# Kernel optimization log

Measured on AMD Instinct MI355X. Metric: run time of the kernel, lower is better.

The kernel has to match this reference:

```python
import jax, jax.numpy as jnp
import numpy as np

B, N, H, FD = 2, 512, 128, 5
NT, SD, L = 3, 4, 3
COPY = 10.0
EPS = 1e-6


def setup_inputs() -> dict:
    key = jax.random.key(0)
    ks = jax.random.split(key, 20)
    node_type = jax.random.randint(ks[0], (B, N, 1), 0, NT).astype(jnp.float32)
    node_state = jax.random.normal(ks[1], (B, N, SD), jnp.float32)
    node_feats = jnp.concatenate([node_type, node_state], axis=-1)  # [B,N,5]
    adj = jax.random.bernoulli(ks[2], 0.05, (B, N, N)).astype(jnp.float32)
    adj = jnp.maximum(adj, adj.transpose(0, 2, 1)) * (1.0 - jnp.eye(N, dtype=jnp.float32))
    scope_node_mask = jax.random.bernoulli(ks[3], 0.5, (B, N)).astype(jnp.float32)
    scope_edge_mask = jax.random.bernoulli(ks[4], 0.5, (B, N, N)).astype(jnp.float32)
    s = 0.02
    p = dict(
        node_feats=node_feats, adj=adj,
        scope_node_mask=scope_node_mask, scope_edge_mask=scope_edge_mask,
        W_in=jax.random.normal(ks[5], (FD, H)) * s, b_in=jnp.zeros((H,)),
        W_mp=jax.random.normal(ks[6], (L, 2 * H, H)) * s, b_mp=jnp.zeros((L, H)),
        Wt1=jax.random.normal(ks[7], (H, H)) * s, bt1=jnp.zeros((H,)),
        Wt2=jax.random.normal(ks[8], (H, NT)) * s, bt2=jnp.zeros((NT,)),
        Ws1=jax.random.normal(ks[9], (H, H)) * s, bs1=jnp.zeros((H,)),
        Ws2=jax.random.normal(ks[10], (H, SD)) * s, bs2=jnp.zeros((SD,)),
        We1=jax.random.normal(ks[11], (4 * H, H)) * s, be1=jnp.zeros((H,)),
        We2=jax.random.normal(ks[12], (H, 3)) * s, be2=jnp.zeros((3,)),
    )
    return p


def _decode_edge_logits(adj, edl, eye):
    probs = jax.nn.softmax(edl, axis=-1)
    p_keep = probs[..., 0]  # EDGE_DELTA_KEEP = 0
    p_add = probs[..., 1]   # EDGE_DELTA_ADD = 1
    cur = (adj > 0.5).astype(edl.dtype)
    p_next = jnp.clip(p_add + p_keep * cur, EPS, 1.0 - EPS)
    el = jnp.log(p_next) - jnp.log1p(-p_next)  # logit
    return jnp.where(eye[None], -1e9, el)


def _forward(node_feats, adj, scope_node_mask, scope_edge_mask,
             W_in, b_in, W_mp, b_mp, Wt1, bt1, Wt2, bt2,
             Ws1, bs1, Ws2, bs2, We1, be1, We2, be2):
    # encoder: input proj + L rounds of [h, adj@h] -> Linear -> ReLU
    h = jax.nn.relu(node_feats @ W_in + b_in)  # [B,N,H]
    for l in range(L):
        msg = jnp.einsum('bij,bjh->bih', adj, h)
        h = jax.nn.relu(jnp.concatenate([h, msg], axis=-1) @ W_mp[l] + b_mp[l])
    # node heads (2-layer MLPs)
    type_local = jax.nn.relu(h @ Wt1 + bt1) @ Wt2 + bt2      # [B,N,NT]
    state_local = jax.nn.relu(h @ Ws1 + bs1) @ Ws2 + bs2     # [B,N,SD]
    # pairwise edge-delta head
    h_i = h[:, :, None, :]
    h_j = h[:, None, :, :]
    pair = jnp.concatenate([
        jnp.broadcast_to(h_i, (B, N, N, H)),
        jnp.broadcast_to(h_j, (B, N, N, H)),
        jnp.abs(h_i - h_j),
        h_i * h_j,
    ], axis=-1)  # [B,N,N,4H]
    edl = jax.nn.relu(pair @ We1 + be1) @ We2 + be2  # [B,N,N,3]
    edl = 0.5 * (edl + edl.transpose(0, 2, 1, 3))
    eye = jnp.eye(N, dtype=bool)
    edl = jnp.where(eye[None, :, :, None], 0.0, edl)
    # merges with copy paths
    cur_type = jnp.clip(node_feats[..., 0].astype(jnp.int32), 0, NT - 1)
    copy_type = jnp.where(jnp.arange(NT) == cur_type[..., None], COPY, -COPY)
    type_full = jnp.where(scope_node_mask[..., None] != 0, type_local, copy_type)
    scope = scope_node_mask[..., None]
    state_full = scope * state_local + (1.0 - scope) * node_feats[..., 1:]
    copy_edl = jnp.broadcast_to(jnp.where(jnp.arange(3) == 0, COPY, -COPY), (B, N, N, 3))
    copy_edl = jnp.where(eye[None, :, :, None], 0.0, copy_edl)
    edl_full = jnp.where(scope_edge_mask[..., None] != 0, edl, copy_edl)
    el_full = _decode_edge_logits(adj, edl_full, eye)
    return type_full, state_full, edl_full, el_full


def reference(node_feats, adj, scope_node_mask, scope_edge_mask,
              W_in, b_in, W_mp, b_mp, Wt1, bt1, Wt2, bt2,
              Ws1, bs1, Ws2, bs2, We1, be1, We2, be2):
    return _forward(node_feats, adj, scope_node_mask, scope_edge_mask,
                    W_in, b_in, W_mp, b_mp, Wt1, bt1, Wt2, bt2,
                    Ws1, bs1, Ws2, bs2, We1, be1, We2, be2)
```

## Files before the change

kernel.cpp:

```cpp
#include <hip/hip_runtime.h>
#include <math.h>

#define B_ 2
#define N_ 512
#define H_ 128
#define NT_ 3
#define SD_ 4
#define FD_ 5

typedef float f32x4 __attribute__((ext_vector_type(4)));
typedef unsigned int u32x4 __attribute__((ext_vector_type(4)));

#define MFMA16(acc, a, b) \
    asm("s_nop 1\n\tv_mfma_f32_16x16x32_bf16 %0, %1, %2, %0" \
        : "+v"(acc) : "v"(a), "v"(b))

#define CVTPK(d, a, b) \
    asm("v_cvt_pk_bf16_f32 %0, %1, %2" : "=v"(d) : "v"(a), "v"(b))

#define CVTPKA(d, a, b) \
    asm("v_cvt_pk_bf16_f32 %0, |%1|, |%2|" : "=v"(d) : "v"(a), "v"(b))

static __device__ inline unsigned rne1(float f) {
    unsigned u = __float_as_uint(f);
    u += 0x7fffu + ((u >> 16) & 1u);
    return u >> 16;
}

__global__ __launch_bounds__(128) void k_input(const float* __restrict__ feats,
                                               const float* __restrict__ W_in,
                                               const float* __restrict__ b_in,
                                               float* __restrict__ hout,
                                               const float* __restrict__ We1,
                                               const float* __restrict__ We2,
                                               unsigned short* __restrict__ wfrag,
                                               unsigned short* __restrict__ wfrag2) {
    int blk = blockIdx.x, tid = threadIdx.x;
    if (blk < B_ * N_) {
        const float* f = feats + (size_t)blk * FD_;
        float acc = b_in[tid];
#pragma unroll
        for (int k = 0; k < FD_; ++k) acc += f[k] * W_in[k * H_ + tid];
        hout[(size_t)blk * H_ + tid] = fmaxf(acc, 0.f);
        return;
    }
    if (blk < B_ * N_ + 32) {
        int t = (blk - B_ * N_) * 128 + tid;
        int lane = t & 63, cg = (t >> 6) & 7, kb = t >> 9;
        int lr = lane & 15, g = lane >> 4;
        int c = cg * 16 + lr;
        unsigned o[4];
#pragma unroll
        for (int p = 0; p < 4; ++p) {
            float a = We1[(size_t)(256 + kb * 32 + 8 * g + 2 * p) * H_ + c];
            float bq = We1[(size_t)(256 + kb * 32 + 8 * g + 2 * p + 1) * H_ + c];
            o[p] = rne1(a) | (rne1(bq) << 16);
        }
        u32x4 v = {o[0], o[1], o[2], o[3]};
        *(u32x4*)(wfrag + (size_t)t * 8) = v;
        return;
    }
    {
        int t = (blk - (B_ * N_ + 32)) * 128 + tid;
        if (t < 256) {
            int kb = t >> 6, lane = t & 63;
            int oc = lane & 15, g = lane >> 4;
            unsigned w[4];
#pragma unroll
            for (int p = 0; p < 4; ++p) {
                int k0 = kb * 32 + g * 8 + 2 * p;
                int k1 = k0 + 1;
                int c0 = ((k0 >> 6) << 6) | ((k0 & 3) << 4) | ((k0 & 63) >> 2);
                int c1 = ((k1 >> 6) << 6) | ((k1 & 3) << 4) | ((k1 & 63) >> 2);
                float v0 = (oc < 3) ? We2[c0 * 3 + oc] : 0.f;
                float v1 = (oc < 3) ? We2[c1 * 3 + oc] : 0.f;
                w[p] = rne1(v0) | (rne1(v1) << 16);
            }
            u32x4 v = {w[0], w[1], w[2], w[3]};
            *(u32x4*)(wfrag2 + (size_t)t * 8) = v;
        }
    }
}

__global__ __launch_bounds__(128) void k_mp(const float* __restrict__ hin,
                                            float* __restrict__ hout,
                                            const float* __restrict__ adj,
                                            const float* __restrict__ Wl,
                                            const float* __restrict__ bl) {
    __shared__ float hi[H_];
    __shared__ float msg[H_];
    __shared__ unsigned short idxs[N_];
    __shared__ float avals[N_];
    __shared__ int cnt2[2];
    int node = blockIdx.x;
    int b = node >> 9;
    int tid = threadIdx.x;
    int w = tid >> 6, lane = tid & 63;
    hi[tid] = hin[(size_t)node * H_ + tid];
    const float* arow = adj + (size_t)node * N_;
    float4 av = ((const float4*)arow)[tid];
    int segbase = w * 256;
    int cum = 0;
#pragma unroll
    for (int q = 0; q < 4; ++q) {
        float a = (&av.x)[q];
        bool pred = (a != 0.f);
        unsigned long long mask = __ballot(pred);
        if (pred) {
            int pos = segbase + cum +
                      (int)__popcll(mask & ((1ull << lane) - 1ull));
            idxs[pos] = (unsigned short)(tid * 4 + q);
            avals[pos] = a;
        }
        cum += (int)__popcll(mask);
    }
    if (lane == 0) cnt2[w] = cum;
    __syncthreads();

    float m = 0.f;
    const float* hb = hin + ((size_t)b * N_) * H_;
    int n0 = cnt2[0], n1 = cnt2[1];
    for (int t = 0; t < n0; ++t)
        m += avals[t] * hb[(size_t)idxs[t] * H_ + tid];
    for (int t = 0; t < n1; ++t)
        m += avals[256 + t] * hb[(size_t)idxs[256 + t] * H_ + tid];
    msg[tid] = m;
    __syncthreads();

    float acc = bl[tid];
#pragma unroll 4
    for (int k = 0; k < H_; ++k) {
        acc += hi[k]  * Wl[(size_t)k * H_ + tid];
        acc += msg[k] * Wl[(size_t)(k + H_) * H_ + tid];
    }
    hout[(size_t)node * H_ + tid] = fmaxf(acc, 0.f);
}

__global__ __launch_bounds__(128) void k_heads(
    const float* __restrict__ h, const float* __restrict__ feats,
    const float* __restrict__ snm,
    const float* __restrict__ Wt1, const float* __restrict__ bt1,
    const float* __restrict__ Wt2, const float* __restrict__ bt2,
    const float* __restrict__ Ws1, const float* __restrict__ bs1,
    const float* __restrict__ Ws2, const float* __restrict__ bs2,
    const float* __restrict__ We1, const float* __restrict__ be1,
    float* __restrict__ Acoef, float* __restrict__ Bcoef,
    unsigned short* __restrict__ hbf,
    float* __restrict__ type_out, float* __restrict__ state_out) {
    __shared__ float hi[H_], hT[H_], hS[H_];
    int node = blockIdx.x, tid = threadIdx.x;
    float hv0 = h[(size_t)node * H_ + tid];
    hi[tid] = hv0;
    hbf[(size_t)node * H_ + tid] = (unsigned short)rne1(hv0);
    __syncthreads();
    float at = bt1[tid], as = bs1[tid], aa = be1[tid], ab = 0.f;
#pragma unroll 4
    for (int k = 0; k < H_; ++k) {
        float hv = hi[k];
        at += hv * Wt1[k * H_ + tid];
        as += hv * Ws1[k * H_ + tid];
        aa += hv * We1[k * H_ + tid];
        ab += hv * We1[(k + H_) * H_ + tid];
    }
    hT[tid] = fmaxf(at, 0.f);
    hS[tid] = fmaxf(as, 0.f);
    int c = tid;
    int kp = ((c >> 6) << 6) | ((c & 15) << 2) | ((c >> 4) & 3);
    Acoef[(size_t)node * H_ + kp] = aa;
    Bcoef[(size_t)node * H_ + kp] = ab;
    __syncthreads();
    float sm = snm[node];
    if (tid < NT_) {
        float tl = bt2[tid];
        for (int cc = 0; cc < H_; ++cc) tl += hT[cc] * Wt2[cc * NT_ + tid];
        int ct = (int)feats[(size_t)node * FD_];
        ct = ct < 0 ? 0 : (ct > NT_ - 1 ? NT_ - 1 : ct);
        float cv = (tid == ct) ? 10.f : -10.f;
        type_out[(size_t)node * NT_ + tid] = (sm != 0.f) ? tl : cv;
    }
    if (tid >= 64 && tid < 64 + SD_) {
        int s = tid - 64;
        float sl = bs2[s];
        for (int cc = 0; cc < H_; ++cc) sl += hS[cc] * Ws2[cc * SD_ + s];
        state_out[(size_t)node * SD_ + s] =
            sm * sl + (1.f - sm) * feats[(size_t)node * FD_ + 1 + s];
    }
}

__global__ __launch_bounds__(256, 2) void k_pair2(
    const float* __restrict__ h, const unsigned short* __restrict__ hbf,
    const float* __restrict__ Acp, const float* __restrict__ Bcp,
    const unsigned short* __restrict__ wfrag,
    const unsigned short* __restrict__ wfrag2,
    const float* __restrict__ be2, const float* __restrict__ sem,
    const float* __restrict__ adj,
    float* __restrict__ edl_out, float* __restrict__ el_out) {

    __shared__ unsigned short tile[2][128][128];

    int bid = blockIdx.x;
    int b = 0, r = bid;
    if (r >= 1280) { b = 1; r -= 1280; }
    int jtile, i;
    if (r < 128)      { jtile = 0; i = r; }
    else if (r < 384) { jtile = 1; i = r - 128; }
    else if (r < 768) { jtile = 2; i = r - 384; }
    else              { jtile = 3; i = r - 768; }
    int JT0 = jtile << 7;
    bool diagblk = (jtile == (i >> 7));
    int bN = b << 9;

    int tid = threadIdx.x;
    int wave = tid >> 6, lane = tid & 63;
    int jh = wave >> 1, ch = wave & 1;
    int lr = lane & 15, g = lane >> 4;

    u32x4 Bf[4][8];
#pragma unroll
    for (int ct = 0; ct < 4; ++ct)
#pragma unroll
        for (int kb = 0; kb < 8; ++kb)
            Bf[ct][kb] = *(const u32x4*)(wfrag +
                (((size_t)kb * 8 + (ch * 4 + ct)) * 64 + lane) * 8);

    const float* hrow = h + (size_t)(bN + i) * H_;
    float him[4][8];
#pragma unroll
    for (int m = 0; m < 4; ++m) {
        float4 a = *(const float4*)(hrow + 32 * m + 8 * g);
        float4 bq = *(const float4*)(hrow + 32 * m + 8 * g + 4);
        him[m][0] = a.x;  him[m][1] = a.y;  him[m][2] = a.z;  him[m][3] = a.w;
        him[m][4] = bq.x; him[m][5] = bq.y; him[m][6] = bq.z; him[m][7] = bq.w;
    }

    f32x4 AcoI = *(const f32x4*)(Acp + (size_t)(bN + i) * H_ + ch * 64 + lr * 4);
    f32x4 BcoI = *(const f32x4*)(Bcp + (size_t)(bN + i) * H_ + ch * 64 + lr * 4);

    char* tb0 = (char*)&tile[0][0][0];
    char* tb1 = (char*)&tile[1][0][0];

#pragma unroll
    for (int jt = 0; jt < 4; ++jt) {
        int jloc0 = jh * 64 + jt * 16;
        const unsigned short* hjp =
            hbf + (size_t)(bN + JT0 + jloc0 + lr) * H_ + 8 * g;
        u32x4 hjall[4];
#pragma unroll
        for (int m = 0; m < 4; ++m)
            hjall[m] = *(const u32x4*)(hjp + 32 * m);

        f32x4 acc0 = {0.f, 0.f, 0.f, 0.f};
        f32x4 acc1 = {0.f, 0.f, 0.f, 0.f};
        f32x4 acc2 = {0.f, 0.f, 0.f, 0.f};
        f32x4 acc3 = {0.f, 0.f, 0.f, 0.f};

#pragma unroll
        for (int m = 0; m < 4; ++m) {
            float hjf[8];
#pragma unroll
            for (int p = 0; p < 4; ++p) {
                unsigned d = hjall[m][p];
                hjf[2 * p]     = __uint_as_float(d << 16);
                hjf[2 * p + 1] = __uint_as_float(d & 0xffff0000u);
            }
            float tt[8], uu[8];
#pragma unroll
            for (int t = 0; t < 8; ++t) {
                tt[t] = him[m][t] - hjf[t];
                uu[t] = him[m][t] * hjf[t];
            }
            unsigned t0, t1, t2, t3, u0, u1, u2, u3;
            CVTPKA(t0, tt[0], tt[1]); CVTPKA(t1, tt[2], tt[3]);
            CVTPKA(t2, tt[4], tt[5]); CVTPKA(t3, tt[6], tt[7]);
            CVTPK(u0, uu[0], uu[1]); CVTPK(u1, uu[2], uu[3]);
            CVTPK(u2, uu[4], uu[5]); CVTPK(u3, uu[6], uu[7]);
            u32x4 tav = {t0, t1, t2, t3};
            u32x4 uav = {u0, u1, u2, u3};
            MFMA16(acc0, tav, Bf[0][m]);
            MFMA16(acc1, tav, Bf[1][m]);
            MFMA16(acc2, tav, Bf[2][m]);
            MFMA16(acc3, tav, Bf[3][m]);
            MFMA16(acc0, uav, Bf[0][4 + m]);
            MFMA16(acc1, uav, Bf[1][4 + m]);
            MFMA16(acc2, uav, Bf[2][4 + m]);
            MFMA16(acc3, uav, Bf[3][4 + m]);
        }
        asm("s_nop 7\n\ts_nop 7\n\ts_nop 3"
            : "+v"(acc0), "+v"(acc1), "+v"(acc2), "+v"(acc3));

#pragma unroll
        for (int rr = 0; rr < 4; ++rr) {
            int jloc = jloc0 + 4 * g + rr;
            size_t jn = (size_t)(bN + JT0 + jloc) * H_ + ch * 64 + lr * 4;
            f32x4 BcJ = *(const f32x4*)(Bcp + jn);
            f32x4 AcJ = *(const f32x4*)(Acp + jn);
            float h10 = fmaxf(acc0[rr] + AcoI[0] + BcJ[0], 0.f);
            float h11 = fmaxf(acc1[rr] + AcoI[1] + BcJ[1], 0.f);
            float h12 = fmaxf(acc2[rr] + AcoI[2] + BcJ[2], 0.f);
            float h13 = fmaxf(acc3[rr] + AcoI[3] + BcJ[3], 0.f);
            float h20 = fmaxf(acc0[rr] + AcJ[0] + BcoI[0], 0.f);
            float h21 = fmaxf(acc1[rr] + AcJ[1] + BcoI[1], 0.f);
            float h22 = fmaxf(acc2[rr] + AcJ[2] + BcoI[2], 0.f);
            float h23 = fmaxf(acc3[rr] + AcJ[3] + BcoI[3], 0.f);
            unsigned w10, w11, w20, w21;
            CVTPK(w10, h10, h11); CVTPK(w11, h12, h13);
            CVTPK(w20, h20, h21); CVTPK(w21, h22, h23);
            int byte = jloc * 256 + ch * 128 + lr * 8;
            byte ^= (jloc & 7) << 4;
            uint2 v1; v1.x = w10; v1.y = w11;
            uint2 v2; v2.x = w20; v2.y = w21;
            *(uint2*)(tb0 + byte) = v1;
            *(uint2*)(tb1 + byte) = v2;
        }
    }

    u32x4 Bf2[4];
#pragma unroll
    for (int kb = 0; kb < 4; ++kb)
        Bf2[kb] = *(const u32x4*)(wfrag2 + ((size_t)kb * 64 + lane) * 8);

    __syncthreads();

    f32x4 pacc0 = {0.f,0.f,0.f,0.f}, pacc1 = {0.f,0.f,0.f,0.f};
    f32x4 pacc2 = {0.f,0.f,0.f,0.f}, pacc3 = {0.f,0.f,0.f,0.f};
#pragma unroll
    for (int p = 0; p < 4; ++p) {
        int f = wave + 4 * p;
        int orient = f >> 3, sub = f & 7;
        char* tb = orient ? tb1 : tb0;
        int jloc = sub * 16 + lr;
#pragma unroll
        for (int kb = 0; kb < 4; ++kb) {
            int byte = jloc * 256 + kb * 64 + g * 16;
            byte ^= (jloc & 7) << 4;
            u32x4 a = *(const u32x4*)(tb + byte);
            if (p == 0) { MFMA16(pacc0, a, Bf2[kb]); }
            else if (p == 1) { MFMA16(pacc1, a, Bf2[kb]); }
            else if (p == 2) { MFMA16(pacc2, a, Bf2[kb]); }
            else { MFMA16(pacc3, a, Bf2[kb]); }
        }
    }
    asm("s_nop 7\n\ts_nop 7\n\ts_nop 3"
        : "+v"(pacc0), "+v"(pacc1), "+v"(pacc2), "+v"(pacc3));
    __syncthreads();

    float* sbuf = (float*)&tile[0][0][0];
    if (lr < 3) {
#pragma unroll
        for (int p = 0; p < 4; ++p) {
            int f = wave + 4 * p;
            int orient = f >> 3, sub = f & 7;
            f32x4 pa = (p == 0) ? pacc0 : (p == 1) ? pacc1 : (p == 2) ? pacc2 : pacc3;
#pragma unroll
            for (int rr = 0; rr < 4; ++rr) {
                int jloc = sub * 16 + 4 * g + rr;
                sbuf[((orient << 7) + jloc) * 3 + lr] = pa[rr];
            }
        }
    }
    __syncthreads();

    {
        int d = tid & 1, jloc = tid >> 1;
        int jg = JT0 + jloc;
        bool skip = diagblk && (jg < i);
        if (!skip) {
            float s0 = 0.5f * (sbuf[jloc * 3 + 0] + sbuf[(128 + jloc) * 3 + 0]) + be2[0];
            float s1 = 0.5f * (sbuf[jloc * 3 + 1] + sbuf[(128 + jloc) * 3 + 1]) + be2[1];
            float s2 = 0.5f * (sbuf[jloc * 3 + 2] + sbuf[(128 + jloc) * 3 + 2]) + be2[2];
            size_t p = d ? ((size_t)(bN + jg) * N_ + i)
                         : ((size_t)(bN + i) * N_ + jg);
            if (jg == i) {
                edl_out[p * 3 + 0] = 0.f;
                edl_out[p * 3 + 1] = 0.f;
                edl_out[p * 3 + 2] = 0.f;
                el_out[p] = -1e9f;
            } else {
                float msk = sem[p];
                float e0 = (msk != 0.f) ? s0 : 10.f;
                float e1 = (msk != 0.f) ? s1 : -10.f;
                float e2 = (msk != 0.f) ? s2 : -10.f;
                edl_out[p * 3 + 0] = e0;
                edl_out[p * 3 + 1] = e1;
                edl_out[p * 3 + 2] = e2;
                float a = adj[p];
                float cur = (a > 0.5f) ? 1.f : 0.f;
                float mx = fmaxf(e0, fmaxf(e1, e2));
                float x0 = expf(e0 - mx), x1 = expf(e1 - mx), x2 = expf(e2 - mx);
                float inv = 1.f / (x0 + x1 + x2);
                float pn = x1 * inv + x0 * inv * cur;
                pn = fminf(fmaxf(pn, 1e-6f), 1.f - 1e-6f);
                el_out[p] = logf(pn) - log1pf(-pn);
            }
        }
    }
}

extern "C" void kernel_launch(void* const* d_in, const int* in_sizes, int n_in,
                              void* d_out, int out_size, void* d_ws,
                              size_t ws_size, hipStream_t stream) {
    const float* feats = (const float*)d_in[0];
    const float* adj   = (const float*)d_in[1];
    const float* snm   = (const float*)d_in[2];
    const float* sem   = (const float*)d_in[3];
    const float* W_in  = (const float*)d_in[4];
    const float* b_in  = (const float*)d_in[5];
    const float* W_mp  = (const float*)d_in[6];
    const float* b_mp  = (const float*)d_in[7];
    const float* Wt1 = (const float*)d_in[8],  *bt1 = (const float*)d_in[9];
    const float* Wt2 = (const float*)d_in[10], *bt2 = (const float*)d_in[11];
    const float* Ws1 = (const float*)d_in[12], *bs1 = (const float*)d_in[13];
    const float* Ws2 = (const float*)d_in[14], *bs2 = (const float*)d_in[15];
    const float* We1 = (const float*)d_in[16], *be1 = (const float*)d_in[17];
    const float* We2 = (const float*)d_in[18], *be2 = (const float*)d_in[19];

    float* out = (float*)d_out;
    float* type_out  = out;
    float* state_out = out + 3072;
    float* edl_out   = out + 7168;
    float* el_out    = out + 7168 + 1572864;

    float* ws = (float*)d_ws;
    float* hA = ws;
    float* hB = ws + 131072;
    float* Bcp = ws + 262144;
    unsigned short* hbf    = (unsigned short*)(ws + 393216);
    unsigned short* wfrag  = (unsigned short*)(ws + 458752);
    unsigned short* wfrag2 = (unsigned short*)(ws + 475136);
    float* Acp = hA;

    k_input<<<B_ * N_ + 34, 128, 0, stream>>>(feats, W_in, b_in, hA,
                                              We1, We2, wfrag, wfrag2);
    k_mp<<<B_ * N_, H_, 0, stream>>>(hA, hB, adj, W_mp + 0 * 2 * H_ * H_, b_mp + 0 * H_);
    k_mp<<<B_ * N_, H_, 0, stream>>>(hB, hA, adj, W_mp + 1 * 2 * H_ * H_, b_mp + 1 * H_);
    k_mp<<<B_ * N_, H_, 0, stream>>>(hA, hB, adj, W_mp + 2 * 2 * H_ * H_, b_mp + 2 * H_);
    k_heads<<<B_ * N_, H_, 0, stream>>>(hB, feats, snm, Wt1, bt1, Wt2, bt2,
                                        Ws1, bs1, Ws2, bs2, We1, be1,
                                        Acp, Bcp, hbf, type_out, state_out);
    k_pair2<<<2560, 256, 0, stream>>>(hB, hbf, Acp, Bcp, wfrag, wfrag2,
                                      be2, sem, adj, edl_out, el_out);
}
```

Baseline: 127.6 us.

## Switch pair kernel to fp16 packed math and smaller 64-wide j-tiles

Converts the pair-edge MLP from bf16 to fp16. The |hi-hj| and hi*hj features are now computed directly with packed f16 multiply and subtract instead of fp32 math followed by bf16 conversion, and MFMAs are issued in groups of four per asm block. The j-tile shrinks from 128 to 64 with a matching triangular block mapping, which halves LDS use and allows 4 blocks per CU. Neighbor coefficient loads are hoisted before the MFMA loop. fp16 has narrower range than bf16 and the feature products are computed at fp16 precision, which risks accuracy, and the smaller tiles add more blocks and redundant weight-fragment loads.

```diff
diff --git a/kernel.cpp b/kernel.cpp
--- a/kernel.cpp
+++ b/kernel.cpp
@@ -1,4 +1,5 @@
 #include <hip/hip_runtime.h>
+#include <hip/hip_fp16.h>
 #include <math.h>
 
 #define B_ 2
@@ -11,20 +12,29 @@
 typedef float f32x4 __attribute__((ext_vector_type(4)));
 typedef unsigned int u32x4 __attribute__((ext_vector_type(4)));
 
-#define MFMA16(acc, a, b) \
-    asm("s_nop 1\n\tv_mfma_f32_16x16x32_bf16 %0, %1, %2, %0" \
+#define MFMA4(a0, a1, a2, a3, av, b0, b1, b2, b3) \
+    asm("s_nop 1\n\t" \
+        "v_mfma_f32_16x16x32_f16 %0, %4, %5, %0\n\t" \
+        "v_mfma_f32_16x16x32_f16 %1, %4, %6, %1\n\t" \
+        "v_mfma_f32_16x16x32_f16 %2, %4, %7, %2\n\t" \
+        "v_mfma_f32_16x16x32_f16 %3, %4, %8, %3" \
+        : "+v"(a0), "+v"(a1), "+v"(a2), "+v"(a3) \
+        : "v"(av), "v"(b0), "v"(b1), "v"(b2), "v"(b3))
+
+#define MFMA16F(acc, a, b) \
+    asm("s_nop 1\n\tv_mfma_f32_16x16x32_f16 %0, %1, %2, %0" \
         : "+v"(acc) : "v"(a), "v"(b))
 
-#define CVTPK(d, a, b) \
-    asm("v_cvt_pk_bf16_f32 %0, %1, %2" : "=v"(d) : "v"(a), "v"(b))
-
-#define CVTPKA(d, a, b) \
-    asm("v_cvt_pk_bf16_f32 %0, |%1|, |%2|" : "=v"(d) : "v"(a), "v"(b))
-
-static __device__ inline unsigned rne1(float f) {
-    unsigned u = __float_as_uint(f);
-    u += 0x7fffu + ((u >> 16) & 1u);
-    return u >> 16;
+#define PKMUL(d, a, b) \
+    asm("v_pk_mul_f16 %0, %1, %2" : "=v"(d) : "v"(a), "v"(b))
+#define PKSUB(d, a, b) \
+    asm("v_pk_add_f16 %0, %1, %2 neg_lo:[0,1] neg_hi:[0,1]" \
+        : "=v"(d) : "v"(a), "v"(b))
+#define CVTPKF16(d, a, b) \
+    asm("v_cvt_pkrtz_f16_f32 %0, %1, %2" : "=v"(d) : "v"(a), "v"(b))
+
+static __device__ inline unsigned short f2h(float f) {
+    return __half_as_ushort(__float2half(f));
 }
 
 __global__ __launch_bounds__(128) void k_input(const float* __restrict__ feats,
@@ -54,7 +64,7 @@
         for (int p = 0; p < 4; ++p) {
             float a = We1[(size_t)(256 + kb * 32 + 8 * g + 2 * p) * H_ + c];
             float bq = We1[(size_t)(256 + kb * 32 + 8 * g + 2 * p + 1) * H_ + c];
-            o[p] = rne1(a) | (rne1(bq) << 16);
+            o[p] = (unsigned)f2h(a) | ((unsigned)f2h(bq) << 16);
         }
         u32x4 v = {o[0], o[1], o[2], o[3]};
         *(u32x4*)(wfrag + (size_t)t * 8) = v;
@@ -74,7 +84,7 @@
                 int c1 = ((k1 >> 6) << 6) | ((k1 & 3) << 4) | ((k1 & 63) >> 2);
                 float v0 = (oc < 3) ? We2[c0 * 3 + oc] : 0.f;
                 float v1 = (oc < 3) ? We2[c1 * 3 + oc] : 0.f;
-                w[p] = rne1(v0) | (rne1(v1) << 16);
+                w[p] = (unsigned)f2h(v0) | ((unsigned)f2h(v1) << 16);
             }
             u32x4 v = {w[0], w[1], w[2], w[3]};
             *(u32x4*)(wfrag2 + (size_t)t * 8) = v;
@@ -145,13 +155,13 @@
     const float* __restrict__ Ws2, const float* __restrict__ bs2,
     const float* __restrict__ We1, const float* __restrict__ be1,
     float* __restrict__ Acoef, float* __restrict__ Bcoef,
-    unsigned short* __restrict__ hbf,
+    unsigned short* __restrict__ hf16,
     float* __restrict__ type_out, float* __restrict__ state_out) {
     __shared__ float hi[H_], hT[H_], hS[H_];
     int node = blockIdx.x, tid = threadIdx.x;
     float hv0 = h[(size_t)node * H_ + tid];
     hi[tid] = hv0;
-    hbf[(size_t)node * H_ + tid] = (unsigned short)rne1(hv0);
+    hf16[(size_t)node * H_ + tid] = f2h(hv0);
     __syncthreads();
     float at = bt1[tid], as = bs1[tid], aa = be1[tid], ab = 0.f;
 #pragma unroll 4
@@ -187,8 +197,8 @@
     }
 }
 
-__global__ __launch_bounds__(256, 2) void k_pair2(
-    const float* __restrict__ h, const unsigned short* __restrict__ hbf,
+__global__ __launch_bounds__(256, 4) void k_pair2(
+    const unsigned short* __restrict__ hf16,
     const float* __restrict__ Acp, const float* __restrict__ Bcp,
     const unsigned short* __restrict__ wfrag,
     const unsigned short* __restrict__ wfrag2,
@@ -196,18 +206,20 @@
     const float* __restrict__ adj,
     float* __restrict__ edl_out, float* __restrict__ el_out) {
 
-    __shared__ unsigned short tile[2][128][128];
+    __shared__ unsigned short tile[2][64][128];
 
     int bid = blockIdx.x;
     int b = 0, r = bid;
-    if (r >= 1280) { b = 1; r -= 1280; }
-    int jtile, i;
-    if (r < 128)      { jtile = 0; i = r; }
-    else if (r < 384) { jtile = 1; i = r - 128; }
-    else if (r < 768) { jtile = 2; i = r - 384; }
-    else              { jtile = 3; i = r - 768; }
-    int JT0 = jtile << 7;
-    bool diagblk = (jtile == (i >> 7));
+    if (r >= 2304) { b = 1; r -= 2304; }
+    int t = 0;
+#pragma unroll
+    for (int s = 0; s < 7; ++s) {
+        int sz = (s + 1) * 64;
+        if (r >= sz && t == s) { r -= sz; t = s + 1; }
+    }
+    int jtile = t, i = r;
+    int JT0 = jtile << 6;
+    bool diagblk = ((i >> 6) == jtile);
     int bN = b << 9;
 
     int tid = threadIdx.x;
@@ -223,15 +235,11 @@
             Bf[ct][kb] = *(const u32x4*)(wfrag +
                 (((size_t)kb * 8 + (ch * 4 + ct)) * 64 + lane) * 8);
 
-    const float* hrow = h + (size_t)(bN + i) * H_;
-    float him[4][8];
-#pragma unroll
-    for (int m = 0; m < 4; ++m) {
-        float4 a = *(const float4*)(hrow + 32 * m + 8 * g);
-        float4 bq = *(const float4*)(hrow + 32 * m + 8 * g + 4);
-        him[m][0] = a.x;  him[m][1] = a.y;  him[m][2] = a.z;  him[m][3] = a.w;
-        him[m][4] = bq.x; him[m][5] = bq.y; him[m][6] = bq.z; him[m][7] = bq.w;
-    }
+    const unsigned short* hirow = hf16 + (size_t)(bN + i) * H_;
+    u32x4 him[4];
+#pragma unroll
+    for (int m = 0; m < 4; ++m)
+        him[m] = *(const u32x4*)(hirow + 32 * m + 8 * g);
 
     f32x4 AcoI = *(const f32x4*)(Acp + (size_t)(bN + i) * H_ + ch * 64 + lr * 4);
     f32x4 BcoI = *(const f32x4*)(Bcp + (size_t)(bN + i) * H_ + ch * 64 + lr * 4);
@@ -240,50 +248,42 @@
     char* tb1 = (char*)&tile[1][0][0];
 
 #pragma unroll
-    for (int jt = 0; jt < 4; ++jt) {
-        int jloc0 = jh * 64 + jt * 16;
+    for (int jt = 0; jt < 2; ++jt) {
+        int jloc0 = jh * 32 + jt * 16;
         const unsigned short* hjp =
-            hbf + (size_t)(bN + JT0 + jloc0 + lr) * H_ + 8 * g;
+            hf16 + (size_t)(bN + JT0 + jloc0 + lr) * H_ + 8 * g;
         u32x4 hjall[4];
 #pragma unroll
         for (int m = 0; m < 4; ++m)
             hjall[m] = *(const u32x4*)(hjp + 32 * m);
-
-        f32x4 acc0 = {0.f, 0.f, 0.f, 0.f};
-        f32x4 acc1 = {0.f, 0.f, 0.f, 0.f};
-        f32x4 acc2 = {0.f, 0.f, 0.f, 0.f};
-        f32x4 acc3 = {0.f, 0.f, 0.f, 0.f};
+        f32x4 BcJv[4], AcJv[4];
+#pragma unroll
+        for (int rr = 0; rr < 4; ++rr) {
+            size_t jn = (size_t)(bN + JT0 + jloc0 + 4 * g + rr) * H_ +
+                        ch * 64 + lr * 4;
+            BcJv[rr] = *(const f32x4*)(Bcp + jn);
+            AcJv[rr] = *(const f32x4*)(Acp + jn);
+        }
+
+        f32x4 acc0 = {0.f,0.f,0.f,0.f}, acc1 = {0.f,0.f,0.f,0.f};
+        f32x4 acc2 = {0.f,0.f,0.f,0.f}, acc3 = {0.f,0.f,0.f,0.f};
 
 #pragma unroll
         for (int m = 0; m < 4; ++m) {
-            float hjf[8];
+            u32x4 tav, uav;
 #pragma unroll
             for (int p = 0; p < 4; ++p) {
-                unsigned d = hjall[m][p];
-                hjf[2 * p]     = __uint_as_float(d << 16);
-                hjf[2 * p + 1] = __uint_as_float(d & 0xffff0000u);
+                unsigned hip_ = him[m][p], hjp_ = hjall[m][p];
+                unsigned u_, d_;
+                PKMUL(u_, hip_, hjp_);
+                PKSUB(d_, hip_, hjp_);
+                uav[p] = u_;
+                tav[p] = d_ & 0x7fff7fffu;
             }
-            float tt[8], uu[8];
-#pragma unroll
-            for (int t = 0; t < 8; ++t) {
-                tt[t] = him[m][t] - hjf[t];
-                uu[t] = him[m][t] * hjf[t];
-            }
-            unsigned t0, t1, t2, t3, u0, u1, u2, u3;
-            CVTPKA(t0, tt[0], tt[1]); CVTPKA(t1, tt[2], tt[3]);
-            CVTPKA(t2, tt[4], tt[5]); CVTPKA(t3, tt[6], tt[7]);
-            CVTPK(u0, uu[0], uu[1]); CVTPK(u1, uu[2], uu[3]);
-            CVTPK(u2, uu[4], uu[5]); CVTPK(u3, uu[6], uu[7]);
-            u32x4 tav = {t0, t1, t2, t3};
-            u32x4 uav = {u0, u1, u2, u3};
-            MFMA16(acc0, tav, Bf[0][m]);
-            MFMA16(acc1, tav, Bf[1][m]);
-            MFMA16(acc2, tav, Bf[2][m]);
-            MFMA16(acc3, tav, Bf[3][m]);
-            MFMA16(acc0, uav, Bf[0][4 + m]);
-            MFMA16(acc1, uav, Bf[1][4 + m]);
-            MFMA16(acc2, uav, Bf[2][4 + m]);
-            MFMA16(acc3, uav, Bf[3][4 + m]);
+            MFMA4(acc0, acc1, acc2, acc3, tav,
+                  Bf[0][m], Bf[1][m], Bf[2][m], Bf[3][m]);
+            MFMA4(acc0, acc1, acc2, acc3, uav,
+                  Bf[0][4 + m], Bf[1][4 + m], Bf[2][4 + m], Bf[3][4 + m]);
         }
         asm("s_nop 7\n\ts_nop 7\n\ts_nop 3"
             : "+v"(acc0), "+v"(acc1), "+v"(acc2), "+v"(acc3));
@@ -291,20 +291,17 @@
 #pragma unroll
         for (int rr = 0; rr < 4; ++rr) {
             int jloc = jloc0 + 4 * g + rr;
-            size_t jn = (size_t)(bN + JT0 + jloc) * H_ + ch * 64 + lr * 4;
-            f32x4 BcJ = *(const f32x4*)(Bcp + jn);
-            f32x4 AcJ = *(const f32x4*)(Acp + jn);
-            float h10 = fmaxf(acc0[rr] + AcoI[0] + BcJ[0], 0.f);
-            float h11 = fmaxf(acc1[rr] + AcoI[1] + BcJ[1], 0.f);
-            float h12 = fmaxf(acc2[rr] + AcoI[2] + BcJ[2], 0.f);
-            float h13 = fmaxf(acc3[rr] + AcoI[3] + BcJ[3], 0.f);
-            float h20 = fmaxf(acc0[rr] + AcJ[0] + BcoI[0], 0.f);
-            float h21 = fmaxf(acc1[rr] + AcJ[1] + BcoI[1], 0.f);
-            float h22 = fmaxf(acc2[rr] + AcJ[2] + BcoI[2], 0.f);
-            float h23 = fmaxf(acc3[rr] + AcJ[3] + BcoI[3], 0.f);
+            float h10 = fmaxf(acc0[rr] + AcoI[0] + BcJv[rr][0], 0.f);
+            float h11 = fmaxf(acc1[rr] + AcoI[1] + BcJv[rr][1], 0.f);
+            float h12 = fmaxf(acc2[rr] + AcoI[2] + BcJv[rr][2], 0.f);
+            float h13 = fmaxf(acc3[rr] + AcoI[3] + BcJv[rr][3], 0.f);
+            float h20 = fmaxf(acc0[rr] + AcJv[rr][0] + BcoI[0], 0.f);
+            float h21 = fmaxf(acc1[rr] + AcJv[rr][1] + BcoI[1], 0.f);
+            float h22 = fmaxf(acc2[rr] + AcJv[rr][2] + BcoI[2], 0.f);
+            float h23 = fmaxf(acc3[rr] + AcJv[rr][3] + BcoI[3], 0.f);
             unsigned w10, w11, w20, w21;
-            CVTPK(w10, h10, h11); CVTPK(w11, h12, h13);
-            CVTPK(w20, h20, h21); CVTPK(w21, h22, h23);
+            CVTPKF16(w10, h10, h11); CVTPKF16(w11, h12, h13);
+            CVTPKF16(w20, h20, h21); CVTPKF16(w21, h22, h23);
             int byte = jloc * 256 + ch * 128 + lr * 8;
             byte ^= (jloc & 7) << 4;
             uint2 v1; v1.x = w10; v1.y = w11;
@@ -322,11 +319,10 @@
     __syncthreads();
 
     f32x4 pacc0 = {0.f,0.f,0.f,0.f}, pacc1 = {0.f,0.f,0.f,0.f};
-    f32x4 pacc2 = {0.f,0.f,0.f,0.f}, pacc3 = {0.f,0.f,0.f,0.f};
-#pragma unroll
-    for (int p = 0; p < 4; ++p) {
+#pragma unroll
+    for (int p = 0; p < 2; ++p) {
         int f = wave + 4 * p;
-        int orient = f >> 3, sub = f & 7;
+        int orient = f >> 2, sub = f & 3;
         char* tb = orient ? tb1 : tb0;
         int jloc = sub * 16 + lr;
 #pragma unroll
@@ -334,40 +330,37 @@
             int byte = jloc * 256 + kb * 64 + g * 16;
             byte ^= (jloc & 7) << 4;
             u32x4 a = *(const u32x4*)(tb + byte);
-            if (p == 0) { MFMA16(pacc0, a, Bf2[kb]); }
-            else if (p == 1) { MFMA16(pacc1, a, Bf2[kb]); }
-            else if (p == 2) { MFMA16(pacc2, a, Bf2[kb]); }
-            else { MFMA16(pacc3, a, Bf2[kb]); }
-        }
-    }
-    asm("s_nop 7\n\ts_nop 7\n\ts_nop 3"
-        : "+v"(pacc0), "+v"(pacc1), "+v"(pacc2), "+v"(pacc3));
+            if (p == 0) { MFMA16F(pacc0, a, Bf2[kb]); }
+            else        { MFMA16F(pacc1, a, Bf2[kb]); }
+        }
+    }
+    asm("s_nop 7\n\ts_nop 7\n\ts_nop 3" : "+v"(pacc0), "+v"(pacc1));
     __syncthreads();
 
     float* sbuf = (float*)&tile[0][0][0];
     if (lr < 3) {
 #pragma unroll
-        for (int p = 0; p < 4; ++p) {
+        for (int p = 0; p < 2; ++p) {
             int f = wave + 4 * p;
-            int orient = f >> 3, sub = f & 7;
-            f32x4 pa = (p == 0) ? pacc0 : (p == 1) ? pacc1 : (p == 2) ? pacc2 : pacc3;
+            int orient = f >> 2, sub = f & 3;
+            f32x4 pa = p ? pacc1 : pacc0;
 #pragma unroll
             for (int rr = 0; rr < 4; ++rr) {
                 int jloc = sub * 16 + 4 * g + rr;
-                sbuf[((orient << 7) + jloc) * 3 + lr] = pa[rr];
+                sbuf[((orient << 6) + jloc) * 3 + lr] = pa[rr];
             }
         }
     }
     __syncthreads();
 
-    {
+    if (tid < 128) {
         int d = tid & 1, jloc = tid >> 1;
         int jg = JT0 + jloc;
         bool skip = diagblk && (jg < i);
         if (!skip) {
-            float s0 = 0.5f * (sbuf[jloc * 3 + 0] + sbuf[(128 + jloc) * 3 + 0]) + be2[0];
-            float s1 = 0.5f * (sbuf[jloc * 3 + 1] + sbuf[(128 + jloc) * 3 + 1]) + be2[1];
-            float s2 = 0.5f * (sbuf[jloc * 3 + 2] + sbuf[(128 + jloc) * 3 + 2]) + be2[2];
+            float s0 = 0.5f * (sbuf[jloc * 3 + 0] + sbuf[(64 + jloc) * 3 + 0]) + be2[0];
+            float s1 = 0.5f * (sbuf[jloc * 3 + 1] + sbuf[(64 + jloc) * 3 + 1]) + be2[1];
+            float s2 = 0.5f * (sbuf[jloc * 3 + 2] + sbuf[(64 + jloc) * 3 + 2]) + be2[2];
             size_t p = d ? ((size_t)(bN + jg) * N_ + i)
                          : ((size_t)(bN + i) * N_ + jg);
             if (jg == i) {
@@ -424,19 +417,22 @@
     float* hA = ws;
     float* hB = ws + 131072;
     float* Bcp = ws + 262144;
-    unsigned short* hbf    = (unsigned short*)(ws + 393216);
+    unsigned short* hf16   = (unsigned short*)(ws + 393216);
     unsigned short* wfrag  = (unsigned short*)(ws + 458752);
     unsigned short* wfrag2 = (unsigned short*)(ws + 475136);
     float* Acp = hA;
 
     k_input<<<B_ * N_ + 34, 128, 0, stream>>>(feats, W_in, b_in, hA,
                                               We1, We2, wfrag, wfrag2);
-    k_mp<<<B_ * N_, H_, 0, stream>>>(hA, hB, adj, W_mp + 0 * 2 * H_ * H_, b_mp + 0 * H_);
-    k_mp<<<B_ * N_, H_, 0, stream>>>(hB, hA, adj, W_mp + 1 * 2 * H_ * H_, b_mp + 1 * H_);
-    k_mp<<<B_ * N_, H_, 0, stream>>>(hA, hB, adj, W_mp + 2 * 2 * H_ * H_, b_mp + 2 * H_);
+    k_mp<<<B_ * N_, H_, 0, stream>>>(hA, hB, adj,
+                                     W_mp + 0 * 2 * H_ * H_, b_mp + 0 * H_);
+    k_mp<<<B_ * N_, H_, 0, stream>>>(hB, hA, adj,
+                                     W_mp + 1 * 2 * H_ * H_, b_mp + 1 * H_);
+    k_mp<<<B_ * N_, H_, 0, stream>>>(hA, hB, adj,
+                                     W_mp + 2 * 2 * H_ * H_, b_mp + 2 * H_);
     k_heads<<<B_ * N_, H_, 0, stream>>>(hB, feats, snm, Wt1, bt1, Wt2, bt2,
                                         Ws1, bs1, Ws2, bs2, We1, be1,
-                                        Acp, Bcp, hbf, type_out, state_out);
-    k_pair2<<<2560, 256, 0, stream>>>(hB, hbf, Acp, Bcp, wfrag, wfrag2,
+                                        Acp, Bcp, hf16, type_out, state_out);
+    k_pair2<<<4608, 256, 0, stream>>>(hf16, Acp, Bcp, wfrag, wfrag2,
                                       be2, sem, adj, edl_out, el_out);
 }
```

Result: slower. 131.2 us (+2.9%).
